# Kernel optimization log

Hardware: AMD Instinct MI355X
Metric: run time of the kernel (lower is better)

## Reference

```python
import jax, jax.numpy as jnp
import numpy as np

INPUT_DIM = 512
HEAD_NUM = 8
ATT_SIZE = 64
EPS = 1e-5


def layer_norm(x, g, b):
    mu = jnp.mean(x, axis=-1, keepdims=True)
    var = jnp.mean(jnp.square(x - mu), axis=-1, keepdims=True)
    return (x - mu) * jax.lax.rsqrt(var + EPS) * g + b


def setup_inputs() -> dict:
    key = jax.random.key(0)
    ks = jax.random.split(key, 10)
    D, H, A = INPUT_DIM, HEAD_NUM, ATT_SIZE
    HA = H * A
    s = lambda fan_in: 1.0 / np.sqrt(fan_in)
    x = jax.random.normal(ks[0], (32, 6, 256, D), dtype=jnp.float32)
    # Linear weights stored as [in, out] so y = x @ W + b (matches torch x @ W.T)
    Wq = jax.random.uniform(ks[1], (D, HA), jnp.float32, -s(D), s(D))
    bq = jnp.zeros((HA,), jnp.float32)
    Wk = jax.random.uniform(ks[2], (D, HA), jnp.float32, -s(D), s(D))
    bk = jnp.zeros((HA,), jnp.float32)
    Wv = jax.random.uniform(ks[3], (D, HA), jnp.float32, -s(D), s(D))
    bv = jnp.zeros((HA,), jnp.float32)
    Wo = jax.random.uniform(ks[4], (HA, D), jnp.float32, -s(HA), s(HA))
    bo = jnp.zeros((D,), jnp.float32)
    g1 = jnp.ones((D,), jnp.float32)
    b1 = jnp.zeros((D,), jnp.float32)
    Wd = jax.random.uniform(ks[5], (2 * D, D), jnp.float32, -s(2 * D), s(2 * D))
    bd = jnp.zeros((D,), jnp.float32)
    g2 = jnp.ones((D,), jnp.float32)
    b2 = jnp.zeros((D,), jnp.float32)
    return dict(x=x, Wq=Wq, bq=bq, Wk=Wk, bk=bk, Wv=Wv, bv=bv,
                Wo=Wo, bo=bo, g1=g1, b1=b1, Wd=Wd, bd=bd, g2=g2, b2=b2)


def reference(x, Wq, bq, Wk, bk, Wv, bv, Wo, bo, g1, b1, Wd, bd, g2, b2):
    B, M, P, D = x.shape
    H, A = HEAD_NUM, ATT_SIZE
    # QKV projections -> [B, M, H, P, A]
    q = (x @ Wq + bq).reshape(B, M, P, H, A).transpose(0, 1, 3, 2, 4)
    k = (x @ Wk + bk).reshape(B, M, P, H, A).transpose(0, 1, 3, 2, 4)
    v = (x @ Wv + bv).reshape(B, M, P, H, A).transpose(0, 1, 3, 2, 4)
    scores = jnp.einsum('bmhqa,bmhka->bmhqk', q, k) / jnp.sqrt(jnp.float32(A))
    attn = jax.nn.softmax(scores, axis=-1)
    z = jnp.einsum('bmhqk,bmhka->bmhqa', attn, v)
    z = z.transpose(0, 1, 3, 2, 4).reshape(B, M, P, H * A)
    z = jax.nn.relu(x + layer_norm(z @ Wo + bo, g1, b1))
    # patch merge (1/2 downsample)
    if P % 2:  # static shape check, fine under jit
        z = jnp.pad(z, ((0, 0), (0, 0), (0, 1), (0, 0)))
    merged = jnp.concatenate([z[:, :, 0::2, :], z[:, :, 1::2, :]], axis=-1)
    out = jax.nn.relu(layer_norm(merged @ Wd + bd, g2, b2))
    return out
```

## Files before the change

### kernel.cpp

```cpp
#include <hip/hip_runtime.h>
#include <hip/hip_bf16.h>
#include <stdint.h>


typedef __hip_bfloat16 bf16;
typedef __attribute__((ext_vector_type(8))) __bf16 bf16v8;
typedef __attribute__((ext_vector_type(4))) float f32x4;
typedef __attribute__((ext_vector_type(8))) short s16x8;
typedef __attribute__((ext_vector_type(4))) short s16x4;

static __device__ __forceinline__ void gl_lds16(const void* src, void* dst) {
  __builtin_amdgcn_global_load_lds((const __attribute__((address_space(1))) void*)src,
                                   (__attribute__((address_space(3))) void*)dst,
                                   16, 0, 0);
}

static __device__ __forceinline__ unsigned short f2bfu(float f) {
  return __builtin_bit_cast(unsigned short, __float2bfloat16(f));
}
static __device__ __forceinline__ float bfu2f(unsigned short u) {
  return __builtin_bit_cast(float, (unsigned int)u << 16);
}

__global__ __launch_bounds__(256) void conv_x_kernel(const float4* __restrict__ x,
                                                     s16x4* __restrict__ xb, int n4) {
  int stride = gridDim.x * 256;
  for (int i = blockIdx.x * 256 + threadIdx.x; i < n4; i += stride) {
    float4 v = x[i];
    s16x4 o;
    o[0] = (short)f2bfu(v.x); o[1] = (short)f2bfu(v.y);
    o[2] = (short)f2bfu(v.z); o[3] = (short)f2bfu(v.w);
    xb[i] = o;
  }
}

__global__ __launch_bounds__(256) void conv_w_kernel(
    const float* __restrict__ Wq, const float* __restrict__ Wk, const float* __restrict__ Wv,
    const float* __restrict__ Wo, const float* __restrict__ Wd,
    const float* __restrict__ bq, const float* __restrict__ bk, const float* __restrict__ bv,
    bf16* __restrict__ wqkv_t, bf16* __restrict__ wo_t, bf16* __restrict__ wd_t,
    float* __restrict__ bqkv) {
  int o = blockIdx.x * 256 + threadIdx.x;
  if (o < 786432) {
    int j = o >> 9, kk = o & 511;
    const float* W = (j < 512) ? Wq : (j < 1024) ? Wk : Wv;
    wqkv_t[o] = __float2bfloat16(W[kk * 512 + (j & 511)]);
  } else if (o < 1048576) {
    int o2 = o - 786432; int j = o2 >> 9, kk = o2 & 511;
    wo_t[o2] = __float2bfloat16(Wo[kk * 512 + j]);
  } else if (o < 1572864) {
    int o3 = o - 1048576; int j = o3 >> 10, kk = o3 & 1023;
    wd_t[o3] = __float2bfloat16(Wd[kk * 512 + j]);
  } else if (o < 1574400) {
    int o4 = o - 1572864;
    const float* b = (o4 < 512) ? bq : (o4 < 1024) ? bk : bv;
    bqkv[o4] = b[o4 & 511];
  }
}

template<int EPI, int AMODE>
__global__ __launch_bounds__(256, 2) void gemm128(
    const bf16* __restrict__ A, const bf16* __restrict__ Bt,
    const float* __restrict__ bias, int K, int nN,
    bf16* __restrict__ oq, bf16* __restrict__ ok, bf16* __restrict__ ovt,
    bf16* __restrict__ obf) {
  __shared__ __align__(16) char smem[65536];
  const int tid = threadIdx.x;
  const int wave = tid >> 6, lane = tid & 63;
  const int wr = wave >> 1, wc = wave & 1;
  const int lane15 = lane & 15, g = lane >> 4;

  const int cpx = gridDim.x >> 3;
  const int lin = (blockIdx.x & 7) * cpx + (blockIdx.x >> 3);
  const int tileM = (lin / nN) * 128, tileN = (lin % nN) * 128;

  const int iters = K >> 7;

  auto stage = [&](int tau, int q) {
    char* dstb = smem + ((tau & 1) << 15) + ((q >> 1) << 14) + ((q & 1) << 13);
#pragma unroll
    for (int u = 0; u < 2; ++u) {
      int slot = u * 256 + tid;
      int r = slot >> 3;
      int c = (slot & 7) ^ (r & 7);
      int kpos = tau * 64 + c * 8;
      if (q < 2) {
        int mr = tileM + ((q & 1) << 6) + r;
        const bf16* s;
        if (AMODE == 0) {
          s = A + (size_t)mr * K + kpos;
        } else {
          int bm = mr >> 7, pp = mr & 127;
          s = A + (size_t)(bm * 256 + pp * 2 + (kpos >> 9)) * 512 + (kpos & 511);
        }
        gl_lds16(s, dstb + slot * 16);
      } else {
        int nr = tileN + ((q & 1) << 6) + r;
        gl_lds16(Bt + (size_t)nr * K + kpos, dstb + slot * 16);
      }
    }
  };

  f32x4 acc[4][4] = {};
  bf16v8 areg[2][2], breg[2][2][2];
  const int swl = (lane15 & 7);

  stage(0, 0); stage(0, 1); stage(0, 2); stage(0, 3);
  stage(1, 0); stage(1, 1);
  asm volatile("s_waitcnt vmcnt(4)" ::: "memory");
  __builtin_amdgcn_s_barrier();

  for (int it = 0; it < iters; ++it) {
    const bool last = (it == iters - 1);
#pragma unroll
    for (int p = 0; p < 8; ++p) {
      const int buf = p >> 2;
      const int mh = (p >> 1) & 1, nh = p & 1;
      char* Ab = smem + (buf << 15);
      char* Bb = Ab + 16384;
      if (nh == 0) {
#pragma unroll
        for (int f = 0; f < 2; ++f) {
          int row = wr * 64 + mh * 32 + f * 16 + lane15;
#pragma unroll
          for (int ks = 0; ks < 2; ++ks)
            areg[f][ks] = *(const bf16v8*)(Ab + row * 128 + (((ks * 4 + g) ^ swl) << 4));
        }
      }
      if ((p & 3) <= 1) {
#pragma unroll
        for (int n = 0; n < 2; ++n) {
          int row = wc * 64 + nh * 32 + n * 16 + lane15;
#pragma unroll
          for (int ks = 0; ks < 2; ++ks)
            breg[nh][n][ks] = *(const bf16v8*)(Bb + row * 128 + (((ks * 4 + g) ^ swl) << 4));
        }
      }
      if (p == 0)      { stage(2 * it + 1, 2); stage(2 * it + 1, 3); }
      else if (p == 3) { if (!last) { stage(2 * it + 2, 0); stage(2 * it + 2, 1); } }
      else if (p == 4) { if (!last) { stage(2 * it + 2, 2); stage(2 * it + 2, 3); } }
      else if (p == 7) { if (!last) { stage(2 * it + 3, 0); stage(2 * it + 3, 1); } }
      __builtin_amdgcn_s_setprio(1);
#pragma unroll
      for (int ks = 0; ks < 2; ++ks)
#pragma unroll
        for (int f = 0; f < 2; ++f)
#pragma unroll
          for (int n = 0; n < 2; ++n)
            acc[mh * 2 + f][nh * 2 + n] = __builtin_amdgcn_mfma_f32_16x16x32_bf16(
                areg[f][ks], breg[nh][n][ks], acc[mh * 2 + f][nh * 2 + n], 0, 0, 0);
      __builtin_amdgcn_s_setprio(0);
      if (p == 2 || p == 6) {
        asm volatile("s_waitcnt lgkmcnt(0)" ::: "memory");
        __builtin_amdgcn_s_barrier();
      } else if (p == 3) {
        if (last) { asm volatile("s_waitcnt vmcnt(0) lgkmcnt(0)" ::: "memory"); }
        else      { asm volatile("s_waitcnt vmcnt(4) lgkmcnt(0)" ::: "memory"); }
        __builtin_amdgcn_s_barrier();
      } else if (p == 7) {
        if (last) { asm volatile("s_waitcnt lgkmcnt(0)" ::: "memory"); }
        else      { asm volatile("s_waitcnt vmcnt(4) lgkmcnt(0)" ::: "memory"); }
        __builtin_amdgcn_s_barrier();
      }
    }
  }

  const int rowstart = tileM + wr * 64;
  if (EPI == 0 && tileN >= 1024) {
    const int cb = tileN + wc * 64;
    const int hh = (cb - 1024) >> 6;
    const int bmq = rowstart >> 8, p0off = rowstart & 255;
    char* slab = smem + wave * 8192;
#pragma unroll
    for (int fm = 0; fm < 4; ++fm) {
#pragma unroll
      for (int fn = 0; fn < 4; ++fn) {
        float bb = bias[cb + fn * 16 + lane15];
        int a = fn * 16 + lane15;
#pragma unroll
        for (int i = 0; i < 4; ++i) {
          int pl = fm * 16 + g * 4 + i;
          *(bf16*)(slab + a * 128 + ((pl * 2) ^ ((a & 7) << 4))) =
              __float2bfloat16(acc[fm][fn][i] + bb);
        }
      }
    }
    asm volatile("" ::: "memory");
    bf16* vdst = ovt + ((size_t)(bmq * 8 + hh) << 14) + p0off;
#pragma unroll
    for (int r = 0; r < 8; ++r) {
      int a = r * 8 + (lane >> 3);
      int ps = lane & 7;
      s16x8 vv = *(const s16x8*)(slab + a * 128 + ((ps * 16) ^ ((a & 7) << 4)));
      *(s16x8*)(vdst + a * 256 + ps * 8) = vv;
    }
  } else {
    char* slab = smem + wave * 8192;
#pragma unroll
    for (int fm = 0; fm < 4; ++fm) {
#pragma unroll
      for (int fn = 0; fn < 4; ++fn) {
        int col = tileN + wc * 64 + fn * 16 + lane15;
        float bb = bias[col];
        int lb = (fn * 16 + lane15) * 2;
#pragma unroll
        for (int i = 0; i < 4; ++i) {
          int pl = fm * 16 + g * 4 + i;
          *(bf16*)(slab + pl * 128 + (lb ^ ((((pl >> 2) & 3)) << 5))) =
              __float2bfloat16(acc[fm][fn][i] + bb);
        }
      }
    }
    asm volatile("" ::: "memory");
    bf16* dst; int ldc2;
    if (EPI == 0) {
      int cb = tileN + wc * 64;
      int hh = (cb >> 6) & 7;
      bf16* base = (cb < 512) ? oq : ok;
      dst = base + (((size_t)((rowstart >> 8) * 8 + hh)) << 14) + (rowstart & 255) * 64;
      ldc2 = 64;
    } else {
      dst = obf + (size_t)rowstart * 512 + tileN + wc * 64;
      ldc2 = 512;
    }
#pragma unroll
    for (int r = 0; r < 8; ++r) {
      int s = r * 64 + lane;
      int pl = s >> 3, sl = s & 7;
      s16x8 vv = *(const s16x8*)(slab + pl * 128 + ((sl * 16) ^ ((((pl >> 2) & 3)) << 5)));
      *(s16x8*)(dst + (size_t)pl * ldc2 + sl * 8) = vv;
    }
  }
}

__global__ __launch_bounds__(256) void attn_kernel(const bf16* __restrict__ q,
                                                   const bf16* __restrict__ k,
                                                   const bf16* __restrict__ vt,
                                                   bf16* __restrict__ z) {
  __shared__ __align__(16) char smem[81920];
  const int tid = threadIdx.x, wave = tid >> 6, lane = tid & 63;
  const int lane15 = lane & 15, g = lane >> 4;
  const int qc = blockIdx.x, hh = blockIdx.y, bm = blockIdx.z;
  const int bh = bm * 8 + hh;
  const bf16* kbase = k + ((size_t)bh << 14);
  const bf16* vbase = vt + ((size_t)bh << 14);
  const bf16* qbase = q + ((size_t)bh << 14) + (qc * 64 + wave * 16) * 64;

#pragma unroll
  for (int i = 0; i < 8; ++i) {
    int s = i * 256 + tid;
    int kr = s >> 3, ksp = s & 7;
    gl_lds16(kbase + kr * 64 + (ksp ^ (kr & 7)) * 8, smem + s * 16);
    int ar = s >> 5, asp = s & 31;
    gl_lds16(vbase + ar * 256 + (asp ^ (ar & 7)) * 8, smem + 32768 + s * 16);
  }
  bf16v8 qf[2];
#pragma unroll
  for (int kk = 0; kk < 2; ++kk)
    qf[kk] = *(const bf16v8*)(qbase + lane15 * 64 + kk * 32 + g * 8);
  __syncthreads();

  f32x4 sacc[16] = {};
#pragma unroll
  for (int tl = 0; tl < 16; ++tl) {
    int key = tl * 16 + lane15;
    int rb = key * 128, swk = (key & 7) << 4;
#pragma unroll
    for (int kk = 0; kk < 2; ++kk) {
      bf16v8 kf = *(const bf16v8*)(smem + rb + (((kk * 4 + g) * 16) ^ swk));
      sacc[tl] = __builtin_amdgcn_mfma_f32_16x16x32_bf16(qf[kk], kf, sacc[tl], 0, 0, 0);
    }
  }

  float mx[4], sm[4], rcp[4];
#pragma unroll
  for (int i = 0; i < 4; ++i) mx[i] = sacc[0][i];
#pragma unroll
  for (int tl = 1; tl < 16; ++tl)
#pragma unroll
    for (int i = 0; i < 4; ++i) mx[i] = fmaxf(mx[i], sacc[tl][i]);
#pragma unroll
  for (int i = 0; i < 4; ++i) {
    mx[i] = fmaxf(mx[i], __shfl_xor(mx[i], 1));
    mx[i] = fmaxf(mx[i], __shfl_xor(mx[i], 2));
    mx[i] = fmaxf(mx[i], __shfl_xor(mx[i], 4));
    mx[i] = fmaxf(mx[i], __shfl_xor(mx[i], 8));
    sm[i] = 0.f;
  }
#pragma unroll
  for (int tl = 0; tl < 16; ++tl)
#pragma unroll
    for (int i = 0; i < 4; ++i) {
      float e = __expf((sacc[tl][i] - mx[i]) * 0.125f);
      sacc[tl][i] = e; sm[i] += e;
    }
#pragma unroll
  for (int i = 0; i < 4; ++i) {
    sm[i] += __shfl_xor(sm[i], 1);
    sm[i] += __shfl_xor(sm[i], 2);
    sm[i] += __shfl_xor(sm[i], 4);
    sm[i] += __shfl_xor(sm[i], 8);
    rcp[i] = 1.0f / sm[i];
  }

  char* pbase = smem + 65536 + wave * 4096;
  f32x4 oacc[4] = {};
#pragma unroll
  for (int h2 = 0; h2 < 2; ++h2) {
#pragma unroll
    for (int t8 = 0; t8 < 8; ++t8) {
      int tl = h2 * 8 + t8;
#pragma unroll
      for (int i = 0; i < 4; ++i) {
        int r = g * 4 + i;
        int c2 = t8 * 16 + lane15;
        *(bf16*)(pbase + r * 256 + ((c2 * 2) ^ ((r & 7) << 4))) =
            __float2bfloat16(sacc[tl][i] * rcp[i]);
      }
    }
    asm volatile("" ::: "memory");
#pragma unroll
    for (int k2 = 0; k2 < 4; ++k2) {
      int ks = h2 * 4 + k2;
      bf16v8 pf = *(const bf16v8*)(pbase + lane15 * 256 +
                                   ((k2 * 64 + g * 16) ^ ((lane15 & 7) << 4)));
#pragma unroll
      for (int at = 0; at < 4; ++at) {
        int a = at * 16 + lane15;
        bf16v8 vf = *(const bf16v8*)(smem + 32768 + a * 512 +
                                     ((ks * 64 + g * 16) ^ ((a & 7) << 4)));
        oacc[at] = __builtin_amdgcn_mfma_f32_16x16x32_bf16(pf, vf, oacc[at], 0, 0, 0);
      }
    }
    asm volatile("" ::: "memory");
  }

  int trow = bm * 256 + qc * 64 + wave * 16;
#pragma unroll
  for (int at = 0; at < 4; ++at)
#pragma unroll
    for (int i = 0; i < 4; ++i)
      z[(size_t)(trow + g * 4 + i) * 512 + hh * 64 + at * 16 + lane15] =
          __float2bfloat16(oacc[at][i]);
}

static __device__ __forceinline__ float wredsum(float v) {
  v += __shfl_xor(v, 1);  v += __shfl_xor(v, 2);  v += __shfl_xor(v, 4);
  v += __shfl_xor(v, 8);  v += __shfl_xor(v, 16); v += __shfl_xor(v, 32);
  return v;
}

__global__ __launch_bounds__(256) void ln_res_kernel(const bf16* __restrict__ y1,
                                                     const float* __restrict__ x,
                                                     const float* __restrict__ g1,
                                                     const float* __restrict__ b1,
                                                     bf16* __restrict__ z2) {
  const int wave = threadIdx.x >> 6, lane = threadIdx.x & 63;
  const int row = blockIdx.x * 4 + wave;
  const size_t base = (size_t)row * 512 + lane * 8;
  s16x8 yv = *(const s16x8*)(y1 + base);
  float f[8];
#pragma unroll
  for (int j = 0; j < 8; ++j) f[j] = bfu2f((unsigned short)yv[j]);
  float s = 0.f, s2 = 0.f;
#pragma unroll
  for (int j = 0; j < 8; ++j) { s += f[j]; s2 += f[j] * f[j]; }
  s = wredsum(s); s2 = wredsum(s2);
  float mu = s * (1.f / 512.f);
  float var = s2 * (1.f / 512.f) - mu * mu;
  float rs = rsqrtf(var + 1e-5f);
  float4 x0 = *(const float4*)(x + base);
  float4 x1 = *(const float4*)(x + base + 4);
  float xa[8] = {x0.x, x0.y, x0.z, x0.w, x1.x, x1.y, x1.z, x1.w};
  float ga[8], ba[8];
#pragma unroll
  for (int j = 0; j < 8; ++j) { ga[j] = g1[lane * 8 + j]; ba[j] = b1[lane * 8 + j]; }
  s16x8 ov;
#pragma unroll
  for (int j = 0; j < 8; ++j) {
    float v = xa[j] + (f[j] - mu) * rs * ga[j] + ba[j];
    ov[j] = (short)f2bfu(fmaxf(v, 0.f));
  }
  *(s16x8*)(z2 + base) = ov;
}

__global__ __launch_bounds__(256) void ln_out_kernel(const bf16* __restrict__ y2,
                                                     const float* __restrict__ g2,
                                                     const float* __restrict__ b2,
                                                     float* __restrict__ out) {
  const int wave = threadIdx.x >> 6, lane = threadIdx.x & 63;
  const int row = blockIdx.x * 4 + wave;
  const size_t base = (size_t)row * 512 + lane * 8;
  s16x8 yv = *(const s16x8*)(y2 + base);
  float f[8];
#pragma unroll
  for (int j = 0; j < 8; ++j) f[j] = bfu2f((unsigned short)yv[j]);
  float s = 0.f, s2 = 0.f;
#pragma unroll
  for (int j = 0; j < 8; ++j) { s += f[j]; s2 += f[j] * f[j]; }
  s = wredsum(s); s2 = wredsum(s2);
  float mu = s * (1.f / 512.f);
  float var = s2 * (1.f / 512.f) - mu * mu;
  float rs = rsqrtf(var + 1e-5f);
  float o[8];
#pragma unroll
  for (int j = 0; j < 8; ++j)
    o[j] = fmaxf((f[j] - mu) * rs * g2[lane * 8 + j] + b2[lane * 8 + j], 0.f);
  float4 w0 = {o[0], o[1], o[2], o[3]};
  float4 w1 = {o[4], o[5], o[6], o[7]};
  *(float4*)(out + base) = w0;
  *(float4*)(out + base + 4) = w1;
}

extern "C" void kernel_launch(void* const* d_in, const int* in_sizes, int n_in,
                              void* d_out, int out_size, void* d_ws, size_t ws_size,
                              hipStream_t stream) {
  const float* x  = (const float*)d_in[0];
  const float* Wq = (const float*)d_in[1];
  const float* bq = (const float*)d_in[2];
  const float* Wk = (const float*)d_in[3];
  const float* bk = (const float*)d_in[4];
  const float* Wv = (const float*)d_in[5];
  const float* bv = (const float*)d_in[6];
  const float* Wo = (const float*)d_in[7];
  const float* bo = (const float*)d_in[8];
  const float* g1 = (const float*)d_in[9];
  const float* b1 = (const float*)d_in[10];
  const float* Wd = (const float*)d_in[11];
  const float* bd = (const float*)d_in[12];
  const float* g2 = (const float*)d_in[13];
  const float* b2 = (const float*)d_in[14];

  char* ws = (char*)d_ws;
  const size_t SEG = 50331648;
  bf16*  xb   = (bf16*)(ws);
  bf16*  qb   = (bf16*)(ws + SEG);
  bf16*  kb   = (bf16*)(ws + 2 * SEG);
  bf16*  vtb  = (bf16*)(ws + 3 * SEG);
  bf16*  wqkv = (bf16*)(ws + 4 * SEG);
  bf16*  wot  = (bf16*)(ws + 4 * SEG + 1572864);
  bf16*  wdt  = (bf16*)(ws + 4 * SEG + 2097152);
  float* bqkv = (float*)(ws + 4 * SEG + 3145728);
  bf16*  zb   = xb;
  bf16*  y1   = qb;
  bf16*  z2   = kb;
  bf16*  y2   = vtb;

  conv_x_kernel<<<4096, 256, 0, stream>>>((const float4*)x, (s16x4*)xb, 25165824 / 4);
  conv_w_kernel<<<6150, 256, 0, stream>>>(Wq, Wk, Wv, Wo, Wd, bq, bk, bv,
                                          wqkv, wot, wdt, bqkv);
  gemm128<0, 0><<<4608, 256, 0, stream>>>(xb, wqkv, bqkv, 512, 12,
                                          qb, kb, vtb, nullptr);
  attn_kernel<<<dim3(4, 8, 192), 256, 0, stream>>>(qb, kb, vtb, zb);
  gemm128<1, 0><<<1536, 256, 0, stream>>>(zb, wot, bo, 512, 4,
                                          nullptr, nullptr, nullptr, y1);
  ln_res_kernel<<<12288, 256, 0, stream>>>(y1, x, g1, b1, z2);
  gemm128<1, 1><<<768, 256, 0, stream>>>(z2, wdt, bd, 1024, 4,
                                         nullptr, nullptr, nullptr, y2);
  ln_out_kernel<<<6144, 256, 0, stream>>>(y2, g2, b2, (float*)d_out);
}
```

Measured before the change: 317.3 us.

## Restructure GEMM into triple-buffered register ping-pong pipeline; read bf16 residual copy

```diff
diff --git a/kernel.cpp b/kernel.cpp
--- a/kernel.cpp
+++ b/kernel.cpp
@@ -23,7 +23,8 @@
 }
 
 __global__ __launch_bounds__(256) void conv_x_kernel(const float4* __restrict__ x,
-                                                     s16x4* __restrict__ xb, int n4) {
+                                                     s16x4* __restrict__ xb,
+                                                     s16x4* __restrict__ xr, int n4) {
   int stride = gridDim.x * 256;
   for (int i = blockIdx.x * 256 + threadIdx.x; i < n4; i += stride) {
     float4 v = x[i];
@@ -31,6 +32,7 @@
     o[0] = (short)f2bfu(v.x); o[1] = (short)f2bfu(v.y);
     o[2] = (short)f2bfu(v.z); o[3] = (short)f2bfu(v.w);
     xb[i] = o;
+    xr[i] = o;
   }
 }
 
@@ -59,12 +61,12 @@
 }
 
 template<int EPI, int AMODE>
-__global__ __launch_bounds__(256, 2) void gemm128(
+__global__ __launch_bounds__(256, 1) void gemm128p(
     const bf16* __restrict__ A, const bf16* __restrict__ Bt,
     const float* __restrict__ bias, int K, int nN,
     bf16* __restrict__ oq, bf16* __restrict__ ok, bf16* __restrict__ ovt,
     bf16* __restrict__ obf) {
-  __shared__ __align__(16) char smem[65536];
+  __shared__ __align__(16) char smem[98304];
   const int tid = threadIdx.x;
   const int wave = tid >> 6, lane = tid & 63;
   const int wr = wave >> 1, wc = wave & 1;
@@ -74,96 +76,88 @@
   const int lin = (blockIdx.x & 7) * cpx + (blockIdx.x >> 3);
   const int tileM = (lin / nN) * 128, tileN = (lin % nN) * 128;
 
-  const int iters = K >> 7;
-
-  auto stage = [&](int tau, int q) {
-    char* dstb = smem + ((tau & 1) << 15) + ((q >> 1) << 14) + ((q & 1) << 13);
-#pragma unroll
-    for (int u = 0; u < 2; ++u) {
-      int slot = u * 256 + tid;
-      int r = slot >> 3;
-      int c = (slot & 7) ^ (r & 7);
-      int kpos = tau * 64 + c * 8;
-      if (q < 2) {
-        int mr = tileM + ((q & 1) << 6) + r;
-        const bf16* s;
-        if (AMODE == 0) {
-          s = A + (size_t)mr * K + kpos;
-        } else {
-          int bm = mr >> 7, pp = mr & 127;
-          s = A + (size_t)(bm * 256 + pp * 2 + (kpos >> 9)) * 512 + (kpos & 511);
-        }
-        gl_lds16(s, dstb + slot * 16);
+  const int T = K >> 6;
+
+  auto stage = [&](int t) {
+    char* rg = smem + (t % 3) * 32768;
+#pragma unroll
+    for (int u = 0; u < 4; ++u) {
+      int s = u * 256 + tid;
+      int r = s >> 3, c = (s & 7) ^ (r & 7);
+      int kpos = t * 64 + c * 8;
+      int mr = tileM + r;
+      const bf16* src;
+      if (AMODE == 0) {
+        src = A + (size_t)mr * K + kpos;
       } else {
-        int nr = tileN + ((q & 1) << 6) + r;
-        gl_lds16(Bt + (size_t)nr * K + kpos, dstb + slot * 16);
+        int bm = mr >> 7, pp = mr & 127;
+        src = A + (size_t)(bm * 256 + pp * 2 + (kpos >> 9)) * 512 + (kpos & 511);
       }
+      gl_lds16(src, rg + s * 16);
+    }
+#pragma unroll
+    for (int u = 0; u < 4; ++u) {
+      int s = u * 256 + tid;
+      int r = s >> 3, c = (s & 7) ^ (r & 7);
+      gl_lds16(Bt + (size_t)(tileN + r) * K + t * 64 + c * 8,
+               rg + 16384 + s * 16);
     }
   };
 
   f32x4 acc[4][4] = {};
-  bf16v8 areg[2][2], breg[2][2][2];
-  const int swl = (lane15 & 7);
-
-  stage(0, 0); stage(0, 1); stage(0, 2); stage(0, 3);
-  stage(1, 0); stage(1, 1);
-  asm volatile("s_waitcnt vmcnt(4)" ::: "memory");
+  bf16v8 aA[4][2], bA[4][2], aB[4][2], bB[4][2];
+
+#define READS(AS, BS, t)                                                          \
+  {                                                                               \
+    char* rg = smem + ((t) % 3) * 32768;                                          \
+    _Pragma("unroll")                                                             \
+    for (int f = 0; f < 4; ++f) {                                                 \
+      int rowa = wr * 64 + f * 16 + lane15;                                       \
+      int rowb = wc * 64 + f * 16 + lane15;                                       \
+      _Pragma("unroll")                                                           \
+      for (int ks = 0; ks < 2; ++ks) {                                            \
+        AS[f][ks] = *(const bf16v8*)(rg + rowa * 128 +                            \
+                                     (((ks * 4 + g) ^ (rowa & 7)) << 4));         \
+        BS[f][ks] = *(const bf16v8*)(rg + 16384 + rowb * 128 +                    \
+                                     (((ks * 4 + g) ^ (rowb & 7)) << 4));         \
+      }                                                                           \
+    }                                                                             \
+  }
+
+#define MFMAS(AS, BS)                                                             \
+  _Pragma("unroll")                                                               \
+  for (int ks = 0; ks < 2; ++ks)                                                  \
+    _Pragma("unroll")                                                             \
+    for (int f = 0; f < 4; ++f)                                                   \
+      _Pragma("unroll")                                                           \
+      for (int n = 0; n < 4; ++n)                                                 \
+        acc[f][n] = __builtin_amdgcn_mfma_f32_16x16x32_bf16(AS[f][ks], BS[n][ks], \
+                                                            acc[f][n], 0, 0, 0);
+
+  stage(0); stage(1); stage(2);
+  asm volatile("s_waitcnt vmcnt(8)" ::: "memory");
   __builtin_amdgcn_s_barrier();
-
-  for (int it = 0; it < iters; ++it) {
-    const bool last = (it == iters - 1);
-#pragma unroll
-    for (int p = 0; p < 8; ++p) {
-      const int buf = p >> 2;
-      const int mh = (p >> 1) & 1, nh = p & 1;
-      char* Ab = smem + (buf << 15);
-      char* Bb = Ab + 16384;
-      if (nh == 0) {
-#pragma unroll
-        for (int f = 0; f < 2; ++f) {
-          int row = wr * 64 + mh * 32 + f * 16 + lane15;
-#pragma unroll
-          for (int ks = 0; ks < 2; ++ks)
-            areg[f][ks] = *(const bf16v8*)(Ab + row * 128 + (((ks * 4 + g) ^ swl) << 4));
-        }
-      }
-      if ((p & 3) <= 1) {
-#pragma unroll
-        for (int n = 0; n < 2; ++n) {
-          int row = wc * 64 + nh * 32 + n * 16 + lane15;
-#pragma unroll
-          for (int ks = 0; ks < 2; ++ks)
-            breg[nh][n][ks] = *(const bf16v8*)(Bb + row * 128 + (((ks * 4 + g) ^ swl) << 4));
-        }
-      }
-      if (p == 0)      { stage(2 * it + 1, 2); stage(2 * it + 1, 3); }
-      else if (p == 3) { if (!last) { stage(2 * it + 2, 0); stage(2 * it + 2, 1); } }
-      else if (p == 4) { if (!last) { stage(2 * it + 2, 2); stage(2 * it + 2, 3); } }
-      else if (p == 7) { if (!last) { stage(2 * it + 3, 0); stage(2 * it + 3, 1); } }
-      __builtin_amdgcn_s_setprio(1);
-#pragma unroll
-      for (int ks = 0; ks < 2; ++ks)
-#pragma unroll
-        for (int f = 0; f < 2; ++f)
-#pragma unroll
-          for (int n = 0; n < 2; ++n)
-            acc[mh * 2 + f][nh * 2 + n] = __builtin_amdgcn_mfma_f32_16x16x32_bf16(
-                areg[f][ks], breg[nh][n][ks], acc[mh * 2 + f][nh * 2 + n], 0, 0, 0);
-      __builtin_amdgcn_s_setprio(0);
-      if (p == 2 || p == 6) {
-        asm volatile("s_waitcnt lgkmcnt(0)" ::: "memory");
-        __builtin_amdgcn_s_barrier();
-      } else if (p == 3) {
-        if (last) { asm volatile("s_waitcnt vmcnt(0) lgkmcnt(0)" ::: "memory"); }
-        else      { asm volatile("s_waitcnt vmcnt(4) lgkmcnt(0)" ::: "memory"); }
-        __builtin_amdgcn_s_barrier();
-      } else if (p == 7) {
-        if (last) { asm volatile("s_waitcnt lgkmcnt(0)" ::: "memory"); }
-        else      { asm volatile("s_waitcnt vmcnt(4) lgkmcnt(0)" ::: "memory"); }
-        __builtin_amdgcn_s_barrier();
-      }
-    }
-  }
+  asm volatile("" ::: "memory");
+  READS(aA, bA, 0);
+
+  const int TP = T >> 1;
+  for (int tp = 0; tp < TP; ++tp) {
+    const int t0 = 2 * tp;
+    READS(aB, bB, t0 + 1);
+    MFMAS(aA, bA);
+    asm volatile("s_waitcnt vmcnt(0)" ::: "memory");
+    __builtin_amdgcn_s_barrier();
+    asm volatile("" ::: "memory");
+    if (t0 + 3 < T) stage(t0 + 3);
+    if (t0 + 2 < T) READS(aA, bA, t0 + 2);
+    MFMAS(aB, bB);
+    asm volatile("s_waitcnt vmcnt(0)" ::: "memory");
+    __builtin_amdgcn_s_barrier();
+    asm volatile("" ::: "memory");
+    if (t0 + 4 < T) stage(t0 + 4);
+  }
+#undef READS
+#undef MFMAS
 
   const int rowstart = tileM + wr * 64;
   if (EPI == 0 && tileN >= 1024) {
@@ -351,7 +345,7 @@
 }
 
 __global__ __launch_bounds__(256) void ln_res_kernel(const bf16* __restrict__ y1,
-                                                     const float* __restrict__ x,
+                                                     const bf16* __restrict__ xr,
                                                      const float* __restrict__ g1,
                                                      const float* __restrict__ b1,
                                                      bf16* __restrict__ z2) {
@@ -359,9 +353,13 @@
   const int row = blockIdx.x * 4 + wave;
   const size_t base = (size_t)row * 512 + lane * 8;
   s16x8 yv = *(const s16x8*)(y1 + base);
-  float f[8];
-#pragma unroll
-  for (int j = 0; j < 8; ++j) f[j] = bfu2f((unsigned short)yv[j]);
+  s16x8 xv = *(const s16x8*)(xr + base);
+  float f[8], xa[8];
+#pragma unroll
+  for (int j = 0; j < 8; ++j) {
+    f[j] = bfu2f((unsigned short)yv[j]);
+    xa[j] = bfu2f((unsigned short)xv[j]);
+  }
   float s = 0.f, s2 = 0.f;
 #pragma unroll
   for (int j = 0; j < 8; ++j) { s += f[j]; s2 += f[j] * f[j]; }
@@ -369,9 +367,6 @@
   float mu = s * (1.f / 512.f);
   float var = s2 * (1.f / 512.f) - mu * mu;
   float rs = rsqrtf(var + 1e-5f);
-  float4 x0 = *(const float4*)(x + base);
-  float4 x1 = *(const float4*)(x + base + 4);
-  float xa[8] = {x0.x, x0.y, x0.z, x0.w, x1.x, x1.y, x1.z, x1.w};
   float ga[8], ba[8];
 #pragma unroll
   for (int j = 0; j < 8; ++j) { ga[j] = g1[lane * 8 + j]; ba[j] = b1[lane * 8 + j]; }
@@ -441,21 +436,23 @@
   bf16*  wot  = (bf16*)(ws + 4 * SEG + 1572864);
   bf16*  wdt  = (bf16*)(ws + 4 * SEG + 2097152);
   float* bqkv = (float*)(ws + 4 * SEG + 3145728);
+  bf16*  xr   = (bf16*)(ws + 4 * SEG + 4194304);
   bf16*  zb   = xb;
   bf16*  y1   = qb;
   bf16*  z2   = kb;
   bf16*  y2   = vtb;
 
-  conv_x_kernel<<<4096, 256, 0, stream>>>((const float4*)x, (s16x4*)xb, 25165824 / 4);
+  conv_x_kernel<<<4096, 256, 0, stream>>>((const float4*)x, (s16x4*)xb,
+                                          (s16x4*)xr, 25165824 / 4);
   conv_w_kernel<<<6150, 256, 0, stream>>>(Wq, Wk, Wv, Wo, Wd, bq, bk, bv,
                                           wqkv, wot, wdt, bqkv);
-  gemm128<0, 0><<<4608, 256, 0, stream>>>(xb, wqkv, bqkv, 512, 12,
-                                          qb, kb, vtb, nullptr);
+  gemm128p<0, 0><<<4608, 256, 0, stream>>>(xb, wqkv, bqkv, 512, 12,
+                                           qb, kb, vtb, nullptr);
   attn_kernel<<<dim3(4, 8, 192), 256, 0, stream>>>(qb, kb, vtb, zb);
-  gemm128<1, 0><<<1536, 256, 0, stream>>>(zb, wot, bo, 512, 4,
-                                          nullptr, nullptr, nullptr, y1);
-  ln_res_kernel<<<12288, 256, 0, stream>>>(y1, x, g1, b1, z2);
-  gemm128<1, 1><<<768, 256, 0, stream>>>(z2, wdt, bd, 1024, 4,
-                                         nullptr, nullptr, nullptr, y2);
+  gemm128p<1, 0><<<1536, 256, 0, stream>>>(zb, wot, bo, 512, 4,
+                                           nullptr, nullptr, nullptr, y1);
+  ln_res_kernel<<<12288, 256, 0, stream>>>(y1, xr, g1, b1, z2);
+  gemm128p<1, 1><<<768, 256, 0, stream>>>(z2, wdt, bd, 1024, 4,
+                                          nullptr, nullptr, nullptr, y2);
   ln_out_kernel<<<6144, 256, 0, stream>>>(y2, g2, b2, (float*)d_out);
 }
```

Result: slower. 418.2 us (+31.8%).

## Process a full head per attention block and keep a bf16 residual copy

Applied to the files above, without the earlier changes.

```diff
diff --git a/kernel.cpp b/kernel.cpp
--- a/kernel.cpp
+++ b/kernel.cpp
@@ -23,7 +23,8 @@
 }
 
 __global__ __launch_bounds__(256) void conv_x_kernel(const float4* __restrict__ x,
-                                                     s16x4* __restrict__ xb, int n4) {
+                                                     s16x4* __restrict__ xb,
+                                                     s16x4* __restrict__ xr, int n4) {
   int stride = gridDim.x * 256;
   for (int i = blockIdx.x * 256 + threadIdx.x; i < n4; i += stride) {
     float4 v = x[i];
@@ -31,6 +32,7 @@
     o[0] = (short)f2bfu(v.x); o[1] = (short)f2bfu(v.y);
     o[2] = (short)f2bfu(v.z); o[3] = (short)f2bfu(v.w);
     xb[i] = o;
+    xr[i] = o;
   }
 }
 
@@ -240,11 +242,10 @@
   __shared__ __align__(16) char smem[81920];
   const int tid = threadIdx.x, wave = tid >> 6, lane = tid & 63;
   const int lane15 = lane & 15, g = lane >> 4;
-  const int qc = blockIdx.x, hh = blockIdx.y, bm = blockIdx.z;
+  const int hh = blockIdx.x, bm = blockIdx.y;
   const int bh = bm * 8 + hh;
   const bf16* kbase = k + ((size_t)bh << 14);
   const bf16* vbase = vt + ((size_t)bh << 14);
-  const bf16* qbase = q + ((size_t)bh << 14) + (qc * 64 + wave * 16) * 64;
 
 #pragma unroll
   for (int i = 0; i < 8; ++i) {
@@ -254,94 +255,99 @@
     int ar = s >> 5, asp = s & 31;
     gl_lds16(vbase + ar * 256 + (asp ^ (ar & 7)) * 8, smem + 32768 + s * 16);
   }
-  bf16v8 qf[2];
-#pragma unroll
-  for (int kk = 0; kk < 2; ++kk)
-    qf[kk] = *(const bf16v8*)(qbase + lane15 * 64 + kk * 32 + g * 8);
   __syncthreads();
 
-  f32x4 sacc[16] = {};
-#pragma unroll
-  for (int tl = 0; tl < 16; ++tl) {
-    int key = tl * 16 + lane15;
-    int rb = key * 128, swk = (key & 7) << 4;
-#pragma unroll
-    for (int kk = 0; kk < 2; ++kk) {
-      bf16v8 kf = *(const bf16v8*)(smem + rb + (((kk * 4 + g) * 16) ^ swk));
-      sacc[tl] = __builtin_amdgcn_mfma_f32_16x16x32_bf16(qf[kk], kf, sacc[tl], 0, 0, 0);
-    }
-  }
-
-  float mx[4], sm[4], rcp[4];
-#pragma unroll
-  for (int i = 0; i < 4; ++i) mx[i] = sacc[0][i];
-#pragma unroll
-  for (int tl = 1; tl < 16; ++tl)
-#pragma unroll
-    for (int i = 0; i < 4; ++i) mx[i] = fmaxf(mx[i], sacc[tl][i]);
-#pragma unroll
-  for (int i = 0; i < 4; ++i) {
-    mx[i] = fmaxf(mx[i], __shfl_xor(mx[i], 1));
-    mx[i] = fmaxf(mx[i], __shfl_xor(mx[i], 2));
-    mx[i] = fmaxf(mx[i], __shfl_xor(mx[i], 4));
-    mx[i] = fmaxf(mx[i], __shfl_xor(mx[i], 8));
-    sm[i] = 0.f;
-  }
-#pragma unroll
-  for (int tl = 0; tl < 16; ++tl)
+  char* pbase = smem + 65536 + wave * 4096;
+
+  for (int fr = 0; fr < 4; ++fr) {
+    const bf16* qbase = q + ((size_t)bh << 14) + (wave * 64 + fr * 16) * 64;
+    bf16v8 qf[2];
+#pragma unroll
+    for (int kk = 0; kk < 2; ++kk)
+      qf[kk] = *(const bf16v8*)(qbase + lane15 * 64 + kk * 32 + g * 8);
+
+    f32x4 sacc[16] = {};
+#pragma unroll
+    for (int tl = 0; tl < 16; ++tl) {
+      int key = tl * 16 + lane15;
+      int rb = key * 128, swk = (key & 7) << 4;
+#pragma unroll
+      for (int kk = 0; kk < 2; ++kk) {
+        bf16v8 kf = *(const bf16v8*)(smem + rb + (((kk * 4 + g) * 16) ^ swk));
+        sacc[tl] = __builtin_amdgcn_mfma_f32_16x16x32_bf16(qf[kk], kf, sacc[tl], 0, 0, 0);
+      }
+    }
+
+    float mx[4], sm[4], rcp[4];
+#pragma unroll
+    for (int i = 0; i < 4; ++i) mx[i] = sacc[0][i];
+#pragma unroll
+    for (int tl = 1; tl < 16; ++tl)
+#pragma unroll
+      for (int i = 0; i < 4; ++i) mx[i] = fmaxf(mx[i], sacc[tl][i]);
 #pragma unroll
     for (int i = 0; i < 4; ++i) {
-      float e = __expf((sacc[tl][i] - mx[i]) * 0.125f);
-      sacc[tl][i] = e; sm[i] += e;
-    }
-#pragma unroll
-  for (int i = 0; i < 4; ++i) {
-    sm[i] += __shfl_xor(sm[i], 1);
-    sm[i] += __shfl_xor(sm[i], 2);
-    sm[i] += __shfl_xor(sm[i], 4);
-    sm[i] += __shfl_xor(sm[i], 8);
-    rcp[i] = 1.0f / sm[i];
-  }
-
-  char* pbase = smem + 65536 + wave * 4096;
-  f32x4 oacc[4] = {};
-#pragma unroll
-  for (int h2 = 0; h2 < 2; ++h2) {
-#pragma unroll
-    for (int t8 = 0; t8 < 8; ++t8) {
-      int tl = h2 * 8 + t8;
+      mx[i] = fmaxf(mx[i], __shfl_xor(mx[i], 1));
+      mx[i] = fmaxf(mx[i], __shfl_xor(mx[i], 2));
+      mx[i] = fmaxf(mx[i], __shfl_xor(mx[i], 4));
+      mx[i] = fmaxf(mx[i], __shfl_xor(mx[i], 8));
+      sm[i] = 0.f;
+    }
+#pragma unroll
+    for (int tl = 0; tl < 16; ++tl)
 #pragma unroll
       for (int i = 0; i < 4; ++i) {
-        int r = g * 4 + i;
-        int c2 = t8 * 16 + lane15;
-        *(bf16*)(pbase + r * 256 + ((c2 * 2) ^ ((r & 7) << 4))) =
-            __float2bfloat16(sacc[tl][i] * rcp[i]);
-      }
-    }
-    asm volatile("" ::: "memory");
-#pragma unroll
-    for (int k2 = 0; k2 < 4; ++k2) {
-      int ks = h2 * 4 + k2;
-      bf16v8 pf = *(const bf16v8*)(pbase + lane15 * 256 +
-                                   ((k2 * 64 + g * 16) ^ ((lane15 & 7) << 4)));
-#pragma unroll
-      for (int at = 0; at < 4; ++at) {
-        int a = at * 16 + lane15;
-        bf16v8 vf = *(const bf16v8*)(smem + 32768 + a * 512 +
-                                     ((ks * 64 + g * 16) ^ ((a & 7) << 4)));
-        oacc[at] = __builtin_amdgcn_mfma_f32_16x16x32_bf16(pf, vf, oacc[at], 0, 0, 0);
-      }
-    }
-    asm volatile("" ::: "memory");
-  }
-
-  int trow = bm * 256 + qc * 64 + wave * 16;
-#pragma unroll
-  for (int at = 0; at < 4; ++at)
-#pragma unroll
-    for (int i = 0; i < 4; ++i)
-      z[(size_t)(trow + g * 4 + i) * 512 + hh * 64 + at * 16 + lane15] =
-          __float2bfloat16(oacc[at][i]);
+        float e = __expf((sacc[tl][i] - mx[i]) * 0.125f);
+        sacc[tl][i] = e; sm[i] += e;
+      }
+#pragma unroll
+    for (int i = 0; i < 4; ++i) {
+      sm[i] += __shfl_xor(sm[i], 1);
+      sm[i] += __shfl_xor(sm[i], 2);
+      sm[i] += __shfl_xor(sm[i], 4);
+      sm[i] += __shfl_xor(sm[i], 8);
+      rcp[i] = 1.0f / sm[i];
+    }
+
+    f32x4 oacc[4] = {};
+#pragma unroll
+    for (int h2 = 0; h2 < 2; ++h2) {
+#pragma unroll
+      for (int t8 = 0; t8 < 8; ++t8) {
+        int tl = h2 * 8 + t8;
+#pragma unroll
+        for (int i = 0; i < 4; ++i) {
+          int r = g * 4 + i;
+          int c2 = t8 * 16 + lane15;
+          *(bf16*)(pbase + r * 256 + ((c2 * 2) ^ ((r & 7) << 4))) =
+              __float2bfloat16(sacc[tl][i] * rcp[i]);
+        }
+      }
+      asm volatile("" ::: "memory");
+#pragma unroll
+      for (int k2 = 0; k2 < 4; ++k2) {
+        int ks = h2 * 4 + k2;
+        bf16v8 pf = *(const bf16v8*)(pbase + lane15 * 256 +
+                                     ((k2 * 64 + g * 16) ^ ((lane15 & 7) << 4)));
+#pragma unroll
+        for (int at = 0; at < 4; ++at) {
+          int a = at * 16 + lane15;
+          bf16v8 vf = *(const bf16v8*)(smem + 32768 + a * 512 +
+                                       ((ks * 64 + g * 16) ^ ((a & 7) << 4)));
+          oacc[at] = __builtin_amdgcn_mfma_f32_16x16x32_bf16(pf, vf, oacc[at], 0, 0, 0);
+        }
+      }
+      asm volatile("" ::: "memory");
+    }
+
+    int trow = bm * 256 + wave * 64 + fr * 16;
+#pragma unroll
+    for (int at = 0; at < 4; ++at)
+#pragma unroll
+      for (int i = 0; i < 4; ++i)
+        z[(size_t)(trow + g * 4 + i) * 512 + hh * 64 + at * 16 + lane15] =
+            __float2bfloat16(oacc[at][i]);
+  }
 }
 
 static __device__ __forceinline__ float wredsum(float v) {
@@ -351,7 +357,7 @@
 }
 
 __global__ __launch_bounds__(256) void ln_res_kernel(const bf16* __restrict__ y1,
-                                                     const float* __restrict__ x,
+                                                     const bf16* __restrict__ xr,
                                                      const float* __restrict__ g1,
                                                      const float* __restrict__ b1,
                                                      bf16* __restrict__ z2) {
@@ -359,9 +365,13 @@
   const int row = blockIdx.x * 4 + wave;
   const size_t base = (size_t)row * 512 + lane * 8;
   s16x8 yv = *(const s16x8*)(y1 + base);
-  float f[8];
-#pragma unroll
-  for (int j = 0; j < 8; ++j) f[j] = bfu2f((unsigned short)yv[j]);
+  s16x8 xv = *(const s16x8*)(xr + base);
+  float f[8], xa[8];
+#pragma unroll
+  for (int j = 0; j < 8; ++j) {
+    f[j] = bfu2f((unsigned short)yv[j]);
+    xa[j] = bfu2f((unsigned short)xv[j]);
+  }
   float s = 0.f, s2 = 0.f;
 #pragma unroll
   for (int j = 0; j < 8; ++j) { s += f[j]; s2 += f[j] * f[j]; }
@@ -369,9 +379,6 @@
   float mu = s * (1.f / 512.f);
   float var = s2 * (1.f / 512.f) - mu * mu;
   float rs = rsqrtf(var + 1e-5f);
-  float4 x0 = *(const float4*)(x + base);
-  float4 x1 = *(const float4*)(x + base + 4);
-  float xa[8] = {x0.x, x0.y, x0.z, x0.w, x1.x, x1.y, x1.z, x1.w};
   float ga[8], ba[8];
 #pragma unroll
   for (int j = 0; j < 8; ++j) { ga[j] = g1[lane * 8 + j]; ba[j] = b1[lane * 8 + j]; }
@@ -441,20 +448,22 @@
   bf16*  wot  = (bf16*)(ws + 4 * SEG + 1572864);
   bf16*  wdt  = (bf16*)(ws + 4 * SEG + 2097152);
   float* bqkv = (float*)(ws + 4 * SEG + 3145728);
+  bf16*  xr   = (bf16*)(ws + 4 * SEG + 4194304);
   bf16*  zb   = xb;
   bf16*  y1   = qb;
   bf16*  z2   = kb;
   bf16*  y2   = vtb;
 
-  conv_x_kernel<<<4096, 256, 0, stream>>>((const float4*)x, (s16x4*)xb, 25165824 / 4);
+  conv_x_kernel<<<4096, 256, 0, stream>>>((const float4*)x, (s16x4*)xb,
+                                          (s16x4*)xr, 25165824 / 4);
   conv_w_kernel<<<6150, 256, 0, stream>>>(Wq, Wk, Wv, Wo, Wd, bq, bk, bv,
                                           wqkv, wot, wdt, bqkv);
   gemm128<0, 0><<<4608, 256, 0, stream>>>(xb, wqkv, bqkv, 512, 12,
                                           qb, kb, vtb, nullptr);
-  attn_kernel<<<dim3(4, 8, 192), 256, 0, stream>>>(qb, kb, vtb, zb);
+  attn_kernel<<<dim3(8, 192), 256, 0, stream>>>(qb, kb, vtb, zb);
   gemm128<1, 0><<<1536, 256, 0, stream>>>(zb, wot, bo, 512, 4,
                                           nullptr, nullptr, nullptr, y1);
-  ln_res_kernel<<<12288, 256, 0, stream>>>(y1, x, g1, b1, z2);
+  ln_res_kernel<<<12288, 256, 0, stream>>>(y1, xr, g1, b1, z2);
   gemm128<1, 1><<<768, 256, 0, stream>>>(z2, wdt, bd, 1024, 4,
                                          nullptr, nullptr, nullptr, y2);
   ln_out_kernel<<<6144, 256, 0, stream>>>(y2, g2, b2, (float*)d_out);
```

New measurement: 300.9 us. -5.1%, faster.

## Fuse fp32-to-bf16 conversion of x into QKV GEMM loads; restructure attention grid

Applied to the files above, without the earlier changes.

```diff
diff --git a/kernel.cpp b/kernel.cpp
--- a/kernel.cpp
+++ b/kernel.cpp
@@ -20,18 +20,6 @@
 }
 static __device__ __forceinline__ float bfu2f(unsigned short u) {
   return __builtin_bit_cast(float, (unsigned int)u << 16);
-}
-
-__global__ __launch_bounds__(256) void conv_x_kernel(const float4* __restrict__ x,
-                                                     s16x4* __restrict__ xb, int n4) {
-  int stride = gridDim.x * 256;
-  for (int i = blockIdx.x * 256 + threadIdx.x; i < n4; i += stride) {
-    float4 v = x[i];
-    s16x4 o;
-    o[0] = (short)f2bfu(v.x); o[1] = (short)f2bfu(v.y);
-    o[2] = (short)f2bfu(v.z); o[3] = (short)f2bfu(v.w);
-    xb[i] = o;
-  }
 }
 
 __global__ __launch_bounds__(256) void conv_w_kernel(
@@ -75,6 +63,7 @@
   const int tileM = (lin / nN) * 128, tileN = (lin % nN) * 128;
 
   const int iters = K >> 7;
+  const float* Xf = (const float*)A;
 
   auto stage = [&](int tau, int q) {
     char* dstb = smem + ((tau & 1) << 15) + ((q >> 1) << 14) + ((q & 1) << 13);
@@ -87,11 +76,11 @@
       if (q < 2) {
         int mr = tileM + ((q & 1) << 6) + r;
         const bf16* s;
-        if (AMODE == 0) {
-          s = A + (size_t)mr * K + kpos;
-        } else {
+        if (AMODE == 1) {
           int bm = mr >> 7, pp = mr & 127;
           s = A + (size_t)(bm * 256 + pp * 2 + (kpos >> 9)) * 512 + (kpos & 511);
+        } else {
+          s = A + (size_t)mr * K + kpos;
         }
         gl_lds16(s, dstb + slot * 16);
       } else {
@@ -105,10 +94,66 @@
   bf16v8 areg[2][2], breg[2][2][2];
   const int swl = (lane15 & 7);
 
-  stage(0, 0); stage(0, 1); stage(0, 2); stage(0, 3);
-  stage(1, 0); stage(1, 1);
-  asm volatile("s_waitcnt vmcnt(4)" ::: "memory");
-  __builtin_amdgcn_s_barrier();
+  f32x4 af[4][2];
+
+#define LOADA_F32(TAU)                                                     \
+  {                                                                        \
+    _Pragma("unroll")                                                      \
+    for (int u = 0; u < 4; ++u) {                                          \
+      int s = u * 256 + tid;                                               \
+      int r = s >> 3, c = (s & 7) ^ (r & 7);                               \
+      const float* src = Xf + (size_t)(tileM + r) * 512 + (TAU) * 64 + c * 8; \
+      af[u][0] = *(const f32x4*)src;                                       \
+      af[u][1] = *(const f32x4*)(src + 4);                                 \
+    }                                                                      \
+  }
+
+#define WRITEA(BASE)                                                       \
+  {                                                                        \
+    _Pragma("unroll")                                                      \
+    for (int u = 0; u < 4; ++u) {                                          \
+      int s = u * 256 + tid;                                               \
+      s16x8 w;                                                             \
+      _Pragma("unroll")                                                    \
+      for (int j = 0; j < 4; ++j) {                                        \
+        w[j]     = (short)f2bfu(af[u][0][j]);                              \
+        w[4 + j] = (short)f2bfu(af[u][1][j]);                              \
+      }                                                                    \
+      *(s16x8*)(smem + (BASE) + s * 16) = w;                               \
+    }                                                                      \
+  }
+
+  if (AMODE == 2) {
+    f32x4 a0[4][2];
+#pragma unroll
+    for (int u = 0; u < 4; ++u) {
+      int s = u * 256 + tid;
+      int r = s >> 3, c = (s & 7) ^ (r & 7);
+      const float* src = Xf + (size_t)(tileM + r) * 512 + c * 8;
+      a0[u][0] = *(const f32x4*)src;
+      a0[u][1] = *(const f32x4*)(src + 4);
+    }
+    stage(0, 2); stage(0, 3);
+    LOADA_F32(1);
+#pragma unroll
+    for (int u = 0; u < 4; ++u) {
+      int s = u * 256 + tid;
+      s16x8 w;
+#pragma unroll
+      for (int j = 0; j < 4; ++j) {
+        w[j]     = (short)f2bfu(a0[u][0][j]);
+        w[4 + j] = (short)f2bfu(a0[u][1][j]);
+      }
+      *(s16x8*)(smem + s * 16) = w;
+    }
+    asm volatile("s_waitcnt vmcnt(8) lgkmcnt(0)" ::: "memory");
+    __builtin_amdgcn_s_barrier();
+  } else {
+    stage(0, 0); stage(0, 1); stage(0, 2); stage(0, 3);
+    stage(1, 0); stage(1, 1);
+    asm volatile("s_waitcnt vmcnt(4)" ::: "memory");
+    __builtin_amdgcn_s_barrier();
+  }
 
   for (int it = 0; it < iters; ++it) {
     const bool last = (it == iters - 1);
@@ -137,9 +182,21 @@
         }
       }
       if (p == 0)      { stage(2 * it + 1, 2); stage(2 * it + 1, 3); }
-      else if (p == 3) { if (!last) { stage(2 * it + 2, 0); stage(2 * it + 2, 1); } }
+      else if (p == 1) { if (AMODE == 2) WRITEA(32768); }
+      else if (p == 3) {
+        if (!last) {
+          if (AMODE == 2) { LOADA_F32(2 * it + 2); }
+          else            { stage(2 * it + 2, 0); stage(2 * it + 2, 1); }
+        }
+      }
       else if (p == 4) { if (!last) { stage(2 * it + 2, 2); stage(2 * it + 2, 3); } }
-      else if (p == 7) { if (!last) { stage(2 * it + 3, 0); stage(2 * it + 3, 1); } }
+      else if (p == 5) { if (AMODE == 2 && !last) WRITEA(0); }
+      else if (p == 7) {
+        if (!last) {
+          if (AMODE == 2) { LOADA_F32(2 * it + 3); }
+          else            { stage(2 * it + 3, 0); stage(2 * it + 3, 1); }
+        }
+      }
       __builtin_amdgcn_s_setprio(1);
 #pragma unroll
       for (int ks = 0; ks < 2; ++ks)
@@ -155,15 +212,19 @@
         __builtin_amdgcn_s_barrier();
       } else if (p == 3) {
         if (last) { asm volatile("s_waitcnt vmcnt(0) lgkmcnt(0)" ::: "memory"); }
+        else if (AMODE == 2) { asm volatile("s_waitcnt vmcnt(8) lgkmcnt(0)" ::: "memory"); }
         else      { asm volatile("s_waitcnt vmcnt(4) lgkmcnt(0)" ::: "memory"); }
         __builtin_amdgcn_s_barrier();
       } else if (p == 7) {
         if (last) { asm volatile("s_waitcnt lgkmcnt(0)" ::: "memory"); }
+        else if (AMODE == 2) { asm volatile("s_waitcnt vmcnt(8) lgkmcnt(0)" ::: "memory"); }
         else      { asm volatile("s_waitcnt vmcnt(4) lgkmcnt(0)" ::: "memory"); }
         __builtin_amdgcn_s_barrier();
       }
     }
   }
+#undef LOADA_F32
+#undef WRITEA
 
   const int rowstart = tileM + wr * 64;
   if (EPI == 0 && tileN >= 1024) {
@@ -240,11 +301,10 @@
   __shared__ __align__(16) char smem[81920];
   const int tid = threadIdx.x, wave = tid >> 6, lane = tid & 63;
   const int lane15 = lane & 15, g = lane >> 4;
-  const int qc = blockIdx.x, hh = blockIdx.y, bm = blockIdx.z;
+  const int hh = blockIdx.x, bm = blockIdx.y;
   const int bh = bm * 8 + hh;
   const bf16* kbase = k + ((size_t)bh << 14);
   const bf16* vbase = vt + ((size_t)bh << 14);
-  const bf16* qbase = q + ((size_t)bh << 14) + (qc * 64 + wave * 16) * 64;
 
 #pragma unroll
   for (int i = 0; i < 8; ++i) {
@@ -254,94 +314,99 @@
     int ar = s >> 5, asp = s & 31;
     gl_lds16(vbase + ar * 256 + (asp ^ (ar & 7)) * 8, smem + 32768 + s * 16);
   }
-  bf16v8 qf[2];
-#pragma unroll
-  for (int kk = 0; kk < 2; ++kk)
-    qf[kk] = *(const bf16v8*)(qbase + lane15 * 64 + kk * 32 + g * 8);
   __syncthreads();
 
-  f32x4 sacc[16] = {};
-#pragma unroll
-  for (int tl = 0; tl < 16; ++tl) {
-    int key = tl * 16 + lane15;
-    int rb = key * 128, swk = (key & 7) << 4;
-#pragma unroll
-    for (int kk = 0; kk < 2; ++kk) {
-      bf16v8 kf = *(const bf16v8*)(smem + rb + (((kk * 4 + g) * 16) ^ swk));
-      sacc[tl] = __builtin_amdgcn_mfma_f32_16x16x32_bf16(qf[kk], kf, sacc[tl], 0, 0, 0);
-    }
-  }
-
-  float mx[4], sm[4], rcp[4];
-#pragma unroll
-  for (int i = 0; i < 4; ++i) mx[i] = sacc[0][i];
-#pragma unroll
-  for (int tl = 1; tl < 16; ++tl)
-#pragma unroll
-    for (int i = 0; i < 4; ++i) mx[i] = fmaxf(mx[i], sacc[tl][i]);
-#pragma unroll
-  for (int i = 0; i < 4; ++i) {
-    mx[i] = fmaxf(mx[i], __shfl_xor(mx[i], 1));
-    mx[i] = fmaxf(mx[i], __shfl_xor(mx[i], 2));
-    mx[i] = fmaxf(mx[i], __shfl_xor(mx[i], 4));
-    mx[i] = fmaxf(mx[i], __shfl_xor(mx[i], 8));
-    sm[i] = 0.f;
-  }
-#pragma unroll
-  for (int tl = 0; tl < 16; ++tl)
+  char* pbase = smem + 65536 + wave * 4096;
+
+  for (int fr = 0; fr < 4; ++fr) {
+    const bf16* qbase = q + ((size_t)bh << 14) + (wave * 64 + fr * 16) * 64;
+    bf16v8 qf[2];
+#pragma unroll
+    for (int kk = 0; kk < 2; ++kk)
+      qf[kk] = *(const bf16v8*)(qbase + lane15 * 64 + kk * 32 + g * 8);
+
+    f32x4 sacc[16] = {};
+#pragma unroll
+    for (int tl = 0; tl < 16; ++tl) {
+      int key = tl * 16 + lane15;
+      int rb = key * 128, swk = (key & 7) << 4;
+#pragma unroll
+      for (int kk = 0; kk < 2; ++kk) {
+        bf16v8 kf = *(const bf16v8*)(smem + rb + (((kk * 4 + g) * 16) ^ swk));
+        sacc[tl] = __builtin_amdgcn_mfma_f32_16x16x32_bf16(qf[kk], kf, sacc[tl], 0, 0, 0);
+      }
+    }
+
+    float mx[4], sm[4], rcp[4];
+#pragma unroll
+    for (int i = 0; i < 4; ++i) mx[i] = sacc[0][i];
+#pragma unroll
+    for (int tl = 1; tl < 16; ++tl)
+#pragma unroll
+      for (int i = 0; i < 4; ++i) mx[i] = fmaxf(mx[i], sacc[tl][i]);
 #pragma unroll
     for (int i = 0; i < 4; ++i) {
-      float e = __expf((sacc[tl][i] - mx[i]) * 0.125f);
-      sacc[tl][i] = e; sm[i] += e;
-    }
-#pragma unroll
-  for (int i = 0; i < 4; ++i) {
-    sm[i] += __shfl_xor(sm[i], 1);
-    sm[i] += __shfl_xor(sm[i], 2);
-    sm[i] += __shfl_xor(sm[i], 4);
-    sm[i] += __shfl_xor(sm[i], 8);
-    rcp[i] = 1.0f / sm[i];
-  }
-
-  char* pbase = smem + 65536 + wave * 4096;
-  f32x4 oacc[4] = {};
-#pragma unroll
-  for (int h2 = 0; h2 < 2; ++h2) {
-#pragma unroll
-    for (int t8 = 0; t8 < 8; ++t8) {
-      int tl = h2 * 8 + t8;
+      mx[i] = fmaxf(mx[i], __shfl_xor(mx[i], 1));
+      mx[i] = fmaxf(mx[i], __shfl_xor(mx[i], 2));
+      mx[i] = fmaxf(mx[i], __shfl_xor(mx[i], 4));
+      mx[i] = fmaxf(mx[i], __shfl_xor(mx[i], 8));
+      sm[i] = 0.f;
+    }
+#pragma unroll
+    for (int tl = 0; tl < 16; ++tl)
 #pragma unroll
       for (int i = 0; i < 4; ++i) {
-        int r = g * 4 + i;
-        int c2 = t8 * 16 + lane15;
-        *(bf16*)(pbase + r * 256 + ((c2 * 2) ^ ((r & 7) << 4))) =
-            __float2bfloat16(sacc[tl][i] * rcp[i]);
-      }
-    }
-    asm volatile("" ::: "memory");
-#pragma unroll
-    for (int k2 = 0; k2 < 4; ++k2) {
-      int ks = h2 * 4 + k2;
-      bf16v8 pf = *(const bf16v8*)(pbase + lane15 * 256 +
-                                   ((k2 * 64 + g * 16) ^ ((lane15 & 7) << 4)));
-#pragma unroll
-      for (int at = 0; at < 4; ++at) {
-        int a = at * 16 + lane15;
-        bf16v8 vf = *(const bf16v8*)(smem + 32768 + a * 512 +
-                                     ((ks * 64 + g * 16) ^ ((a & 7) << 4)));
-        oacc[at] = __builtin_amdgcn_mfma_f32_16x16x32_bf16(pf, vf, oacc[at], 0, 0, 0);
-      }
-    }
-    asm volatile("" ::: "memory");
-  }
-
-  int trow = bm * 256 + qc * 64 + wave * 16;
-#pragma unroll
-  for (int at = 0; at < 4; ++at)
-#pragma unroll
-    for (int i = 0; i < 4; ++i)
-      z[(size_t)(trow + g * 4 + i) * 512 + hh * 64 + at * 16 + lane15] =
-          __float2bfloat16(oacc[at][i]);
+        float e = __expf((sacc[tl][i] - mx[i]) * 0.125f);
+        sacc[tl][i] = e; sm[i] += e;
+      }
+#pragma unroll
+    for (int i = 0; i < 4; ++i) {
+      sm[i] += __shfl_xor(sm[i], 1);
+      sm[i] += __shfl_xor(sm[i], 2);
+      sm[i] += __shfl_xor(sm[i], 4);
+      sm[i] += __shfl_xor(sm[i], 8);
+      rcp[i] = 1.0f / sm[i];
+    }
+
+    f32x4 oacc[4] = {};
+#pragma unroll
+    for (int h2 = 0; h2 < 2; ++h2) {
+#pragma unroll
+      for (int t8 = 0; t8 < 8; ++t8) {
+        int tl = h2 * 8 + t8;
+#pragma unroll
+        for (int i = 0; i < 4; ++i) {
+          int r = g * 4 + i;
+          int c2 = t8 * 16 + lane15;
+          *(bf16*)(pbase + r * 256 + ((c2 * 2) ^ ((r & 7) << 4))) =
+              __float2bfloat16(sacc[tl][i] * rcp[i]);
+        }
+      }
+      asm volatile("" ::: "memory");
+#pragma unroll
+      for (int k2 = 0; k2 < 4; ++k2) {
+        int ks = h2 * 4 + k2;
+        bf16v8 pf = *(const bf16v8*)(pbase + lane15 * 256 +
+                                     ((k2 * 64 + g * 16) ^ ((lane15 & 7) << 4)));
+#pragma unroll
+        for (int at = 0; at < 4; ++at) {
+          int a = at * 16 + lane15;
+          bf16v8 vf = *(const bf16v8*)(smem + 32768 + a * 512 +
+                                       ((ks * 64 + g * 16) ^ ((a & 7) << 4)));
+          oacc[at] = __builtin_amdgcn_mfma_f32_16x16x32_bf16(pf, vf, oacc[at], 0, 0, 0);
+        }
+      }
+      asm volatile("" ::: "memory");
+    }
+
+    int trow = bm * 256 + wave * 64 + fr * 16;
+#pragma unroll
+    for (int at = 0; at < 4; ++at)
+#pragma unroll
+      for (int i = 0; i < 4; ++i)
+        z[(size_t)(trow + g * 4 + i) * 512 + hh * 64 + at * 16 + lane15] =
+            __float2bfloat16(oacc[at][i]);
+  }
 }
 
 static __device__ __forceinline__ float wredsum(float v) {
@@ -359,6 +424,8 @@
   const int row = blockIdx.x * 4 + wave;
   const size_t base = (size_t)row * 512 + lane * 8;
   s16x8 yv = *(const s16x8*)(y1 + base);
+  f32x4 x0 = *(const f32x4*)(x + base);
+  f32x4 x1 = *(const f32x4*)(x + base + 4);
   float f[8];
 #pragma unroll
   for (int j = 0; j < 8; ++j) f[j] = bfu2f((unsigned short)yv[j]);
@@ -369,9 +436,7 @@
   float mu = s * (1.f / 512.f);
   float var = s2 * (1.f / 512.f) - mu * mu;
   float rs = rsqrtf(var + 1e-5f);
-  float4 x0 = *(const float4*)(x + base);
-  float4 x1 = *(const float4*)(x + base + 4);
-  float xa[8] = {x0.x, x0.y, x0.z, x0.w, x1.x, x1.y, x1.z, x1.w};
+  float xa[8] = {x0[0], x0[1], x0[2], x0[3], x1[0], x1[1], x1[2], x1[3]};
   float ga[8], ba[8];
 #pragma unroll
   for (int j = 0; j < 8; ++j) { ga[j] = g1[lane * 8 + j]; ba[j] = b1[lane * 8 + j]; }
@@ -433,7 +498,7 @@
 
   char* ws = (char*)d_ws;
   const size_t SEG = 50331648;
-  bf16*  xb   = (bf16*)(ws);
+  bf16*  zb   = (bf16*)(ws);
   bf16*  qb   = (bf16*)(ws + SEG);
   bf16*  kb   = (bf16*)(ws + 2 * SEG);
   bf16*  vtb  = (bf16*)(ws + 3 * SEG);
@@ -441,17 +506,15 @@
   bf16*  wot  = (bf16*)(ws + 4 * SEG + 1572864);
   bf16*  wdt  = (bf16*)(ws + 4 * SEG + 2097152);
   float* bqkv = (float*)(ws + 4 * SEG + 3145728);
-  bf16*  zb   = xb;
   bf16*  y1   = qb;
   bf16*  z2   = kb;
   bf16*  y2   = vtb;
 
-  conv_x_kernel<<<4096, 256, 0, stream>>>((const float4*)x, (s16x4*)xb, 25165824 / 4);
   conv_w_kernel<<<6150, 256, 0, stream>>>(Wq, Wk, Wv, Wo, Wd, bq, bk, bv,
                                           wqkv, wot, wdt, bqkv);
-  gemm128<0, 0><<<4608, 256, 0, stream>>>(xb, wqkv, bqkv, 512, 12,
+  gemm128<0, 2><<<4608, 256, 0, stream>>>((const bf16*)x, wqkv, bqkv, 512, 12,
                                           qb, kb, vtb, nullptr);
-  attn_kernel<<<dim3(4, 8, 192), 256, 0, stream>>>(qb, kb, vtb, zb);
+  attn_kernel<<<dim3(8, 192), 256, 0, stream>>>(qb, kb, vtb, zb);
   gemm128<1, 0><<<1536, 256, 0, stream>>>(zb, wot, bo, 512, 4,
                                           nullptr, nullptr, nullptr, y1);
   ln_res_kernel<<<12288, 256, 0, stream>>>(y1, x, g1, b1, z2);
```

Measured after the change: 328.1 us. +3.4%, slower.
